# Performance work log

Measured on AMD Instinct MI355X. Metric: run time of the kernel, lower is better.

## Reference

```python
import jax, jax.numpy as jnp
import numpy as np

H = 768        # spanbert_out
WF = 20        # width_encoding_feature_size
MSW = 10       # max_span_width
TOP_RATIO = 0.4
MAX_ANTE = 50
DEPTH = 2      # coref_depth
D = 3 * H + WF # span_rep_size = 2324
NEG = -1e30


def setup_inputs() -> dict:
    key = jax.random.key(0)
    ks = jax.random.split(key, 12)
    W, G = 2048, 100
    seq = jax.random.normal(ks[0], (W, H), jnp.float32)
    sentence_map = jnp.sort(jax.random.randint(ks[1], (W,), 0, 64))
    gold_starts = jax.random.randint(ks[2], (G,), 0, W)
    gold_ends = jnp.clip(gold_starts + jax.random.randint(ks[3], (G,), 0, MSW), 0, W - 1)
    cluster_ids = jax.random.randint(ks[4], (G,), 0, 20)
    s = 0.02
    return {
        "sequence_output": seq,
        "W_alpha": jax.random.normal(ks[5], (H, 1), jnp.float32) * s,
        "b_alpha": jnp.zeros((1,), jnp.float32),
        "W_m": jax.random.normal(ks[6], (D, 1), jnp.float32) * s,
        "b_m": jnp.zeros((1,), jnp.float32),
        "W_c": jax.random.normal(ks[7], (D, D), jnp.float32) * s,
        "W_a": jax.random.normal(ks[8], (3 * D, 1), jnp.float32) * s,
        "b_a": jnp.zeros((1,), jnp.float32),
        "W_f": jax.random.normal(ks[9], (2 * D, D), jnp.float32) * s,
        "b_f": jnp.zeros((D,), jnp.float32),
        "width_feats": jax.random.normal(ks[10], (MSW, WF), jnp.float32) * s,
        "sentence_map": sentence_map,
        "gold_starts": gold_starts,
        "gold_ends": gold_ends,
        "cluster_ids": cluster_ids,
    }


def _forward(seq, W_alpha, b_alpha, W_m, b_m, W_c, W_a, b_a, W_f, b_f, width_feats,
             sentence_map, gold_starts, gold_ends, cluster_ids):
    W = seq.shape[0]
    # candidate spans: [W, MSW] -> flat [N], N = W*MSW
    cs = jnp.broadcast_to(jnp.arange(W)[:, None], (W, MSW)).reshape(-1)
    ce = (jnp.arange(W)[:, None] + jnp.arange(MSW)[None, :]).reshape(-1)
    ce_c = jnp.minimum(ce, W - 1)
    valid = (ce < W) & (sentence_map[cs] == sentence_map[ce_c])  # [N]

    # candidate cluster labels (get_candidate_labels): sum cluster ids of exact gold matches
    same_span = (cs[:, None] == gold_starts[None, :]) & (ce_c[:, None] == gold_ends[None, :])
    cand_cluster = jnp.sum(jnp.where(same_span, cluster_ids[None, :], 0), axis=1)  # [N]

    # span representations
    start_emb = seq[cs]                               # [N,H]
    end_emb = seq[ce_c]                               # [N,H]
    alphas = (seq @ W_alpha + b_alpha)[:, 0]          # [W]
    doc_range = jnp.arange(W)[None, :]
    mmask = (doc_range >= cs[:, None]) & (doc_range <= ce_c[:, None])  # [N,W]
    attn = jax.nn.softmax(jnp.where(mmask, alphas[None, :], NEG), axis=1)
    span_emb = attn @ seq                             # [N,H]
    widths = jnp.clip(ce_c - cs, 0, MSW - 1)          # width - 1
    rep = jnp.concatenate([start_emb, end_emb, span_emb, width_feats[widths]], axis=1)  # [N,D]

    # mention scoring + top-m pruning (masked_select replaced by -inf masking)
    mention_scores = (rep @ W_m + b_m)[:, 0]          # [N]
    masked_scores = jnp.where(valid, mention_scores, NEG)
    m = int(TOP_RATIO * W)
    _, top_idx = jax.lax.top_k(masked_scores, m)
    top_idx = jnp.sort(top_idx)
    top_rep = rep[top_idx]                            # [m,D]
    ts, te = cs[top_idx], ce_c[top_idx]
    tscore = mention_scores[top_idx]
    tcluster = cand_cluster[top_idx]

    # prune antecedents
    k = min(m, MAX_ANTE)
    offsets = jnp.arange(m)[:, None] - jnp.arange(m)[None, :]
    amask = offsets >= 1
    fast = tscore[:, None] + tscore[None, :] + jnp.where(amask, 0.0, NEG)
    fast = fast + (top_rep @ W_c) @ top_rep.T         # [m,m]
    _, top_ante = jax.lax.top_k(fast, k)              # [m,k]
    ta_mask = jnp.take_along_axis(amask, top_ante, axis=1)
    ta_fast = jnp.take_along_axis(fast, top_ante, axis=1)

    # iterative attention-weighted antecedent aggregation with gated update
    dummy = jnp.zeros((m, 1), seq.dtype)
    reps = top_rep
    scores_a = ta_fast
    for _ in range(DEPTH):
        ante_emb = reps[top_ante]                     # [m,k,D]
        tgt = reps[:, None, :]
        pair = jnp.concatenate(
            [jnp.broadcast_to(tgt, (m, k, D)), ante_emb, ante_emb * tgt], axis=2)  # [m,k,3D]
        slow = (pair @ W_a)[:, :, 0] + b_a[0]         # [m,k]
        scores_a = ta_fast + slow
        wts = jax.nn.softmax(jnp.concatenate([dummy, scores_a], axis=1), axis=1)  # [m,k+1]
        full = jnp.concatenate([reps[:, None, :], ante_emb], axis=1)              # [m,k+1,D]
        attended = jnp.sum(wts[:, :, None] * full, axis=1)                        # [m,D]
        f = jax.nn.sigmoid(jnp.concatenate([reps, attended], axis=1) @ W_f + b_f)
        reps = f * attended + (1.0 - f) * reps

    final_scores = jnp.concatenate([dummy, scores_a], axis=1)  # [m,k+1]

    # antecedent labels and marginal log-likelihood loss
    ante_cluster = jnp.where(ta_mask, tcluster[top_ante], -1)
    pairwise = (ante_cluster == tcluster[:, None]) & (tcluster > 0)[:, None]
    dummy_lab = ~jnp.any(pairwise, axis=1, keepdims=True)
    lab = jnp.concatenate([dummy_lab, pairwise], axis=1)
    gold_scores = jnp.where(lab, final_scores, NEG)
    loss = jnp.sum(jax.nn.logsumexp(final_scores, axis=1) - jax.nn.logsumexp(gold_scores, axis=1))
    return ts, te, top_ante, final_scores, loss


def reference(sequence_output, W_alpha, b_alpha, W_m, b_m, W_c, W_a, b_a, W_f, b_f,
              width_feats, sentence_map, gold_starts, gold_ends, cluster_ids):
    return _forward(sequence_output, W_alpha, b_alpha, W_m, b_m, W_c, W_a, b_a,
                    W_f, b_f, width_feats, sentence_map, gold_starts, gold_ends, cluster_ids)
```

## Files before the change

kernel.cpp:

```cpp
#include <hip/hip_runtime.h>
#include <cfloat>
#include <climits>
#include <math.h>

#define HD   768
#define MSW  10
#define WFK  20
#define DD   2324
#define K2   50
#define NEGF (-1e30f)

#define KPAD 2432
#define KAW  4864
#define MPAD 896
#define NPAD 2432

typedef __attribute__((ext_vector_type(8))) short    s8b;
typedef __attribute__((ext_vector_type(8))) unsigned short u16x8;
typedef __attribute__((ext_vector_type(4))) float    f32x4;

__device__ inline unsigned short f2bf(float f){
  unsigned u = __float_as_uint(f);
  unsigned r = (u + 0x7FFFu + ((u >> 16) & 1u)) >> 16;
  return (unsigned short)r;
}
__device__ inline float bf2f(unsigned short h){
  return __uint_as_float(((unsigned)h) << 16);
}

__device__ __forceinline__ void gload16(const unsigned short* g, void* l){
  __builtin_amdgcn_global_load_lds(
      (const __attribute__((address_space(1))) void*)g,
      (__attribute__((address_space(3))) void*)l, 16, 0, 0);
}

__device__ __forceinline__ int swz_col(int row, int col){
  return col ^ ((row & 7) << 3);
}

__device__ __forceinline__ void xcd_remap(int &bx, int &by, int &bz){
  int nwg  = (int)(gridDim.x*gridDim.y*gridDim.z);
  int orig = (int)(blockIdx.x + gridDim.x*(blockIdx.y + gridDim.y*blockIdx.z));
  int q = nwg >> 3, r = nwg & 7;
  int x8 = orig & 7, o8 = orig >> 3;
  int wg = (x8 < r ? x8*(q+1) : r*(q+1) + (x8-r)*q) + o8;
  bx = wg % (int)gridDim.x;
  int tmp = wg / (int)gridDim.x;
  by = tmp % (int)gridDim.y;
  bz = tmp / (int)gridDim.y;
}

__global__ void row_proj(const float* __restrict__ seq, const float* __restrict__ Wa,
                         const float* __restrict__ ba, const float* __restrict__ Wm,
                         float* alphas, float* p1, float* p2, float* p3, int W){
  int w = blockIdx.x; int tid = threadIdx.x;
  const float* row = seq + (size_t)w * HD;
  float s0=0.f, s1=0.f, s2=0.f, s3=0.f;
  for(int h=tid; h<HD; h+=256){
    float x = row[h];
    s0 += x * Wa[h];
    s1 += x * Wm[h];
    s2 += x * Wm[HD + h];
    s3 += x * Wm[2*HD + h];
  }
  __shared__ float r0[256], r1[256], r2[256], r3[256];
  r0[tid]=s0; r1[tid]=s1; r2[tid]=s2; r3[tid]=s3;
  __syncthreads();
  for(int st=128; st>0; st>>=1){
    if(tid<st){ r0[tid]+=r0[tid+st]; r1[tid]+=r1[tid+st]; r2[tid]+=r2[tid+st]; r3[tid]+=r3[tid+st]; }
    __syncthreads();
  }
  if(tid==0){ alphas[w]=r0[0]+ba[0]; p1[w]=r1[0]; p2[w]=r2[0]; p3[w]=r3[0]; }
}

__global__ void mention_kernel(const float* __restrict__ alphas, const float* __restrict__ p1,
                               const float* __restrict__ p2, const float* __restrict__ p3,
                               const float* __restrict__ wfeat, const float* __restrict__ Wm,
                               const float* __restrict__ bm,
                               const int* __restrict__ smap, const int* __restrict__ gs,
                               const int* __restrict__ ge, const int* __restrict__ cid, int G,
                               float* mscore, float* mmask, int* ccl, int W){
  int c = blockIdx.x*blockDim.x + threadIdx.x;
  int C = W * MSW;
  if(c >= C) return;
  int s = c / MSW, r = c - s*MSW;
  int e = s + r; int ec = min(e, W-1);
  int L = ec - s;
  bool valid = (e < W) && (smap[s] == smap[ec]);
  float maxa = -FLT_MAX;
  for(int j=0;j<=L;j++) maxa = fmaxf(maxa, alphas[s+j]);
  float sum=0.f, sdot=0.f;
  for(int j=0;j<=L;j++){ float ee = expf(alphas[s+j]-maxa); sum += ee; sdot += ee*p3[s+j]; }
  sdot /= sum;
  float wp=0.f;
  for(int f=0; f<WFK; f++) wp += wfeat[L*WFK+f] * Wm[3*HD+f];
  float ms = p1[s] + p2[ec] + sdot + wp + bm[0];
  mscore[c] = ms;
  mmask[c]  = valid ? ms : NEGF;
  int cc = 0;
  for(int g=0; g<G; g++) if(s==gs[g] && ec==ge[g]) cc += cid[g];
  ccl[c] = cc;
}

__device__ inline unsigned fkey(float f){
  unsigned b = __float_as_uint(f);
  return (b & 0x80000000u) ? ~b : (b | 0x80000000u);
}

__global__ __launch_bounds__(1024)
void select_kernel(const float* __restrict__ mmask, const float* __restrict__ mscore,
                   const int* __restrict__ ccl, int m, int C, int W,
                   int* top_idx, float* tscore, int* tclust,
                   float* out_ts, float* out_te){
  const int T = 1024;
  int tid = threadIdx.x;
  int chunk = (C + T - 1)/T;
  int lo = tid*chunk, hi = min(lo+chunk, C);
  int n = hi - lo; if(n < 0) n = 0;
  unsigned kb[32];
  for(int t=0;t<n;t++) kb[t] = fkey(mmask[lo+t]);

  __shared__ unsigned s_hist[256];
  __shared__ unsigned s_scan[1024];
  __shared__ unsigned s_pref;
  __shared__ int s_rem;
  if(tid==0){ s_pref=0u; s_rem=m; }
  __syncthreads();

  for(int b=3;b>=0;b--){
    if(tid<256) s_hist[tid]=0u;
    __syncthreads();
    unsigned pref = s_pref;
    unsigned msk = (b==3)?0u:(0xFFFFFFFFu << ((b+1)*8));
    for(int t=0;t<n;t++){
      unsigned u = kb[t];
      if((u & msk)==pref) atomicAdd(&s_hist[(u>>(b*8))&0xFFu], 1u);
    }
    __syncthreads();
    if(tid==0){
      int rem = s_rem; unsigned acc=0u; int bin;
      for(bin=255;bin>=1;bin--){
        unsigned h = s_hist[bin];
        if(acc + h >= (unsigned)rem) break;
        acc += h;
      }
      if(bin < 0) bin = 0;
      s_pref = pref | ((unsigned)bin << (b*8));
      s_rem = rem - (int)acc;
    }
    __syncthreads();
  }
  unsigned Tk = s_pref;
  int need = s_rem;

  unsigned nG=0, nE=0;
  for(int t=0;t<n;t++){ unsigned u=kb[t]; nG += (u>Tk)?1u:0u; nE += (u==Tk)?1u:0u; }

  s_scan[tid]=nE; __syncthreads();
  for(int off=1; off<T; off<<=1){
    unsigned x = (tid>=off)? s_scan[tid-off]:0u; __syncthreads();
    s_scan[tid]+=x; __syncthreads();
  }
  unsigned eqBase = s_scan[tid]-nE;
  __syncthreads();

  int takeLeft = need - (int)eqBase;
  int take = takeLeft<0?0:(takeLeft>(int)nE?(int)nE:takeLeft);
  unsigned selCnt = nG + (unsigned)take;

  s_scan[tid]=selCnt; __syncthreads();
  for(int off=1; off<T; off<<=1){
    unsigned x = (tid>=off)? s_scan[tid-off]:0u; __syncthreads();
    s_scan[tid]+=x; __syncthreads();
  }
  unsigned posBase = s_scan[tid]-selCnt;

  int pos = (int)posBase; int eq = (int)eqBase;
  for(int t=0;t<n;t++){
    unsigned u = kb[t];
    bool sel = false;
    if(u>Tk) sel=true;
    else if(u==Tk){ if(eq<need) sel=true; eq++; }
    if(sel){
      int c = lo+t;
      top_idx[pos] = c;
      int s = c/MSW, r = c - s*MSW; int e = min(s + r, W-1);
      tscore[pos] = mscore[c];
      tclust[pos] = ccl[c];
      out_ts[pos] = (float)s;
      out_te[pos] = (float)e;
      pos++;
    }
  }
}

__global__ void build_rep(const float* __restrict__ seq, const float* __restrict__ alphas,
                          const float* __restrict__ wfeat, const int* __restrict__ top_idx,
                          float* rep, int W){
  int i = blockIdx.x; int tid = threadIdx.x;
  int c = top_idx[i];
  int s = c/MSW, r = c - s*MSW; int ec = min(s + r, W-1); int L = ec - s;
  float wv[MSW];
  float maxa = -FLT_MAX;
  for(int j=0;j<=L;j++) maxa = fmaxf(maxa, alphas[s+j]);
  float sum = 0.f;
  for(int j=0;j<=L;j++){ wv[j] = expf(alphas[s+j]-maxa); sum += wv[j]; }
  float inv = 1.f/sum;
  float* o = rep + (size_t)i*DD;
  for(int d=tid; d<HD; d+=256){
    o[d]      = seq[(size_t)s*HD + d];
    o[HD+d]   = seq[(size_t)ec*HD + d];
    float sp = 0.f;
    for(int j=0;j<=L;j++) sp += wv[j]*seq[(size_t)(s+j)*HD + d];
    o[2*HD+d] = sp*inv;
  }
  for(int f=tid; f<WFK; f+=256) o[3*HD+f] = wfeat[L*WFK+f];
}

__global__ void conv_split(const float* __restrict__ src, int rows, int cols,
                           unsigned short* __restrict__ hi, unsigned short* __restrict__ lo,
                           float* __restrict__ ztgt, int zn){
  int idx = blockIdx.x*256 + threadIdx.x;
  if(idx >= MPAD*KPAD) return;
  if(idx < zn) ztgt[idx] = 0.f;
  int row = idx / KPAD, col = idx - row*KPAD;
  float v = (row < rows && col < cols) ? src[(size_t)row*cols + col] : 0.f;
  unsigned short h = f2bf(v);
  int w = row*KPAD + swz_col(row, col);
  hi[w] = h;
  lo[w] = f2bf(v - bf2f(h));
}

__global__ void conv_split_wcT(const float* __restrict__ Wc,
                               unsigned short* __restrict__ WtH, unsigned short* __restrict__ WtL){
  int n  = blockIdx.y*64 + threadIdx.x;
  int k8 = blockIdx.x*8;
  u16x8 vh, vl;
  #pragma unroll
  for(int j=0;j<8;j++){
    int k = k8 + j;
    float f = (n < DD && k < DD) ? Wc[(size_t)k*DD + n] : 0.f;
    unsigned short h = f2bf(f);
    vh[j] = h;
    vl[j] = f2bf(f - bf2f(h));
  }
  int k8s = swz_col(n, k8);
  *(u16x8*)(WtH + (size_t)n*KPAD + k8s) = vh;
  *(u16x8*)(WtL + (size_t)n*KPAD + k8s) = vl;
}

__global__ __launch_bounds__(256,2)
void gemm_split3_sk(const unsigned short* __restrict__ Ah, const unsigned short* __restrict__ Al,
                    const unsigned short* __restrict__ Bth, const unsigned short* __restrict__ Btl,
                    float* __restrict__ C, int M, int N, int ldc){
  __shared__ __align__(16) unsigned short sAh[128*64];
  __shared__ __align__(16) unsigned short sAl[128*64];
  __shared__ __align__(16) unsigned short sBh[128*64];
  __shared__ __align__(16) unsigned short sBl[128*64];
  int bx, by, bz; xcd_remap(bx, by, bz);
  int t = threadIdx.x;
  int row0 = by*128, col0 = bx*128;
  const int tiles = KPAD/64;
  int per = (tiles + (int)gridDim.z - 1)/(int)gridDim.z;
  int tb = min(bz*per, tiles), te = min(tb + per, tiles);
  if(tb >= te) return;
  int lane = t&63, w = t>>6;
  int wr = (w>>1)*64, wc = (w&1)*64;
  int quad = lane>>4, l15 = lane&15;
  int seg = lane&7;
  size_t ro = (size_t)(w*8 + (lane>>3));
  const unsigned short* gAh = Ah  + ((size_t)row0 + ro)*KPAD + seg*8;
  const unsigned short* gAl = Al  + ((size_t)row0 + ro)*KPAD + seg*8;
  const unsigned short* gBh = Bth + ((size_t)col0 + ro)*KPAD + seg*8;
  const unsigned short* gBl = Btl + ((size_t)col0 + ro)*KPAD + seg*8;
  const int lds0 = (w*8)*64;
  const int c0 = ((quad ^ (l15 & 7)) << 3);

  f32x4 acc[4][4];
  #pragma unroll
  for(int mi=0;mi<4;mi++)
    #pragma unroll
    for(int ni=0;ni<4;ni++) acc[mi][ni] = (f32x4){0.f,0.f,0.f,0.f};

  for(int kt=tb; kt<te; ++kt){
    size_t k0 = (size_t)kt*64;
    #pragma unroll
    for(int r=0;r<4;r++){
      size_t go = (size_t)(r*32)*KPAD + k0;
      int lo = lds0 + r*32*64;
      gload16(gAh + go, sAh + lo);
      gload16(gAl + go, sAl + lo);
      gload16(gBh + go, sBh + lo);
      gload16(gBl + go, sBl + lo);
    }
    __syncthreads();
    #pragma unroll
    for(int ks=0;ks<2;ks++){
      const int co = c0 ^ (ks<<5);
      s8b fah[4], fal[4], fbh[4], fbl[4];
      #pragma unroll
      for(int mi=0;mi<4;mi++){
        int ra = (wr+mi*16+l15)*64 + co;
        fah[mi] = *(const s8b*)&sAh[ra];
        fal[mi] = *(const s8b*)&sAl[ra];
      }
      #pragma unroll
      for(int ni=0;ni<4;ni++){
        int rb = (wc+ni*16+l15)*64 + co;
        fbh[ni] = *(const s8b*)&sBh[rb];
        fbl[ni] = *(const s8b*)&sBl[rb];
      }
      #pragma unroll
      for(int mi=0;mi<4;mi++)
        #pragma unroll
        for(int ni=0;ni<4;ni++){
          acc[mi][ni] = __builtin_amdgcn_mfma_f32_16x16x32_bf16(fah[mi], fbh[ni], acc[mi][ni], 0,0,0);
          acc[mi][ni] = __builtin_amdgcn_mfma_f32_16x16x32_bf16(fah[mi], fbl[ni], acc[mi][ni], 0,0,0);
          acc[mi][ni] = __builtin_amdgcn_mfma_f32_16x16x32_bf16(fal[mi], fbh[ni], acc[mi][ni], 0,0,0);
        }
    }
    __syncthreads();
  }

  #pragma unroll
  for(int ni=0;ni<4;ni++){
    int gn = col0 + wc + ni*16 + l15;
    if(gn >= N) continue;
    #pragma unroll
    for(int mi=0;mi<4;mi++){
      #pragma unroll
      for(int rg=0;rg<4;rg++){
        int gr = row0 + wr + mi*16 + quad*4 + rg;
        if(gr >= M) continue;
        atomicAdd(&C[(size_t)gr*ldc + gn], acc[mi][ni][rg]);
      }
    }
  }
}

__global__ __launch_bounds__(256,2)
void gemm_bf16_m97(const unsigned short* __restrict__ A, const unsigned short* __restrict__ Bt,
                   float* __restrict__ C, int M, int N, int ldc, int ldk, int tiles){
  __shared__ __align__(16) unsigned short sA[2][128*64];
  __shared__ __align__(16) unsigned short sB[2][128*64];
  int bx, by, bz; xcd_remap(bx, by, bz);
  int t = threadIdx.x;
  int row0 = by*128, col0 = bx*128;
  int per = (tiles + (int)gridDim.z - 1)/(int)gridDim.z;
  int tb = min(bz*per, tiles), te = min(tb + per, tiles);
  if(tb >= te) return;
  int lane = t&63, w = t>>6;
  int wr = (w>>1)*64, wc = (w&1)*64;
  int quad = lane>>4, l15 = lane&15;
  int seg = lane&7;
  size_t ro = (size_t)(w*8 + (lane>>3));
  const unsigned short* gA = A  + ((size_t)row0 + ro)*ldk + seg*8;
  const unsigned short* gB = Bt + ((size_t)col0 + ro)*ldk + seg*8;
  const int lds0 = (w*8)*64;
  const int c0 = ((quad ^ (l15 & 7)) << 3);

  f32x4 acc[4][4];
  #pragma unroll
  for(int mi=0;mi<4;mi++)
    #pragma unroll
    for(int ni=0;ni<4;ni++) acc[mi][ni] = (f32x4){0.f,0.f,0.f,0.f};

  auto STAGE = [&](int b, int kt){
    size_t k0 = (size_t)kt*64;
    #pragma unroll
    for(int r=0;r<4;r++){
      size_t go = (size_t)(r*32)*ldk + k0;
      int lo = lds0 + r*32*64;
      gload16(gA + go, &sA[b][lo]);
      gload16(gB + go, &sB[b][lo]);
    }
  };

  STAGE(0, tb);
  __syncthreads();
  int buf = 0;
  for(int kt=tb; kt<te; ++kt){
    if(kt+1 < te) STAGE(buf^1, kt+1);
    #pragma unroll
    for(int ks=0;ks<2;ks++){
      const int co = c0 ^ (ks<<5);
      s8b fa[4], fb[4];
      #pragma unroll
      for(int mi=0;mi<4;mi++) fa[mi] = *(const s8b*)&sA[buf][(wr+mi*16+l15)*64 + co];
      #pragma unroll
      for(int ni=0;ni<4;ni++) fb[ni] = *(const s8b*)&sB[buf][(wc+ni*16+l15)*64 + co];
      #pragma unroll
      for(int mi=0;mi<4;mi++)
        #pragma unroll
        for(int ni=0;ni<4;ni++)
          acc[mi][ni] = __builtin_amdgcn_mfma_f32_16x16x32_bf16(fa[mi], fb[ni], acc[mi][ni], 0,0,0);
    }
    __syncthreads();
    buf ^= 1;
  }

  #pragma unroll
  for(int ni=0;ni<4;ni++){
    int gn = col0 + wc + ni*16 + l15;
    if(gn >= N) continue;
    #pragma unroll
    for(int mi=0;mi<4;mi++){
      #pragma unroll
      for(int rg=0;rg<4;rg++){
        int gr = row0 + wr + mi*16 + quad*4 + rg;
        if(gr >= M) continue;
        atomicAdd(&C[(size_t)gr*ldc + gn], acc[mi][ni][rg]);
      }
    }
  }
}

#define NT 13
__global__ void topante_kernel(const float* __restrict__ tscore, const float* __restrict__ bilin,
                               int m, int* ante, float* tafast, float* out_ante){
  int i = blockIdx.x; int lane = threadIdx.x;
  float tsi = tscore[i];
  float v[NT];
  #pragma unroll
  for(int t=0;t<NT;t++){
    int j = lane + t*64;
    float f = -FLT_MAX;
    if(j < m){
      f = tsi + tscore[j];
      f += (j < i) ? 0.f : NEGF;
      f += bilin[(size_t)i*m + j];
    }
    v[t] = f;
  }
  unsigned consumed = 0u;
  int r_ante = 0; float r_fast = 0.f;
  for(int it=0; it<K2; ++it){
    float lv = -FLT_MAX; int li = m;
    #pragma unroll
    for(int t=0;t<NT;t++){
      bool live = ((consumed >> t) & 1u) == 0u;
      if(live && v[t] > lv){ lv = v[t]; li = lane + t*64; }
    }
    float bv = lv; int bi = li;
    #pragma unroll
    for(int off=32; off>0; off>>=1){
      float ov = __shfl_xor(bv, off);
      int   oi = __shfl_xor(bi, off);
      if(ov > bv || (ov == bv && oi < bi)){ bv = ov; bi = oi; }
    }
    if(bi < m && (bi & 63) == lane) consumed |= (1u << (bi >> 6));
    if(lane == it){ r_ante = bi; r_fast = bv; }
  }
  if(lane < K2){
    ante[(size_t)i*K2 + lane]   = r_ante;
    tafast[(size_t)i*K2 + lane] = r_fast;
    out_ante[(size_t)i*K2+lane] = (float)r_ante;
  }
}

__global__ void uv_kernel(const float* __restrict__ reps, const float* __restrict__ Wa3,
                          float* u, float* v, int m){
  int i = blockIdx.x; int tid = threadIdx.x;
  const float* rp = reps + (size_t)i*DD;
  float s1=0.f, s2=0.f;
  for(int d=tid; d<DD; d+=256){ float x = rp[d]; s1 += x*Wa3[d]; s2 += x*Wa3[DD+d]; }
  __shared__ float r1[256], r2[256];
  r1[tid]=s1; r2[tid]=s2; __syncthreads();
  for(int st=128; st>0; st>>=1){
    if(tid<st){ r1[tid]+=r1[tid+st]; r2[tid]+=r2[tid+st]; }
    __syncthreads();
  }
  if(tid==0){ u[i]=r1[0]; v[i]=r2[0]; }
}

__global__ __launch_bounds__(256)
void slow_dots(const float* __restrict__ cur, const float* __restrict__ Wa3,
               const float* __restrict__ u, const float* __restrict__ v,
               const int* __restrict__ ante, const float* __restrict__ tafast,
               const float* __restrict__ ba, float* __restrict__ sc, int m){
  int i  = blockIdx.y;
  int tq = blockIdx.x;
  int tid = threadIdx.x;
  int lane = tid & 63, w = tid >> 6;
  __shared__ __align__(16) float xi[DD];
  const float* ri = cur + (size_t)i*DD;
  for(int k=tid; k<DD; k+=256) xi[k] = ri[k]*Wa3[2*DD + k];
  __syncthreads();
  const float ui = u[i], b0 = ba[0];
  const int D4 = DD/4;
  const f32x4* xi4 = (const f32x4*)xi;
  int t0 = tq*10;
  for(int t=t0+w; t<t0+10; t+=4){
    int j = ante[(size_t)i*K2 + t];
    const f32x4* rj4 = (const f32x4*)(cur + (size_t)j*DD);
    float s = 0.f;
    for(int k=lane; k<D4; k+=64){
      f32x4 a = xi4[k], b = rj4[k];
      s += a[0]*b[0] + a[1]*b[1] + a[2]*b[2] + a[3]*b[3];
    }
    #pragma unroll
    for(int off=32; off>0; off>>=1) s += __shfl_xor(s, off);
    if(lane==0)
      sc[(size_t)i*K2 + t] = tafast[(size_t)i*K2 + t] + ui + v[j] + s + b0;
  }
}

__global__ __launch_bounds__(256)
void attend_d(const float* __restrict__ cur, const float* __restrict__ sc,
              const int* __restrict__ ante, float* __restrict__ att, int m){
  int i  = blockIdx.y;
  int ch = blockIdx.x;
  int tid = threadIdx.x;
  __shared__ float wts[K2+1];
  __shared__ float scs[K2];
  __shared__ int   js[K2];
  if(tid < K2){ scs[tid] = sc[(size_t)i*K2 + tid]; js[tid] = ante[(size_t)i*K2 + tid]; }
  __syncthreads();
  if(tid==0){
    float mx = 0.f;
    for(int t=0;t<K2;t++) mx = fmaxf(mx, scs[t]);
    float sum = expf(0.f - mx); wts[0] = sum;
    for(int t=0;t<K2;t++){ float e = expf(scs[t]-mx); wts[t+1]=e; sum += e; }
    float inv = 1.f/sum;
    for(int t=0;t<=K2;t++) wts[t] *= inv;
  }
  __syncthreads();
  const int D4 = DD/4;
  const int C4 = 146;
  int d4 = ch*C4 + tid;
  if(tid < C4 && d4 < D4){
    const f32x4* ri4 = (const f32x4*)(cur + (size_t)i*DD);
    f32x4 a = ri4[d4];
    float w0 = wts[0];
    a[0]*=w0; a[1]*=w0; a[2]*=w0; a[3]*=w0;
    for(int t=0;t<K2;t++){
      const f32x4* rj4 = (const f32x4*)(cur + (size_t)js[t]*DD);
      f32x4 b = rj4[d4];
      float wt = wts[t+1];
      a[0]+=wt*b[0]; a[1]+=wt*b[1]; a[2]+=wt*b[2]; a[3]+=wt*b[3];
    }
    ((f32x4*)(att + (size_t)i*DD))[d4] = a;
  }
}

__global__ void conv_acat(const float* __restrict__ cur, const float* __restrict__ att,
                          unsigned short* __restrict__ A,
                          float* __restrict__ nxt, int total, int m){
  int idx = blockIdx.x*256 + threadIdx.x;
  if(idx >= MPAD*KAW) return;
  if(idx < total) nxt[idx] = 0.f;
  int row = idx / KAW, col = idx - row*KAW;
  float v = 0.f;
  if(row < m){
    if(col < DD) v = cur[(size_t)row*DD + col];
    else if(col >= KPAD && col < KPAD + DD) v = att[(size_t)row*DD + (col - KPAD)];
  }
  A[row*KAW + swz_col(row, col)] = f2bf(v);
}

__global__ void conv_wf(const float* __restrict__ Wf, unsigned short* __restrict__ Bt){
  int n  = blockIdx.y*64 + threadIdx.x;
  int k8 = blockIdx.x*8;
  int s  = (k8 >= KPAD) ? 1 : 0;
  int kk = k8 - s*KPAD;
  u16x8 v;
  #pragma unroll
  for(int j=0;j<8;j++){
    int k = kk + j;
    float f = (n < DD && k < DD) ? Wf[(size_t)(s*DD + k)*DD + n] : 0.f;
    v[j] = f2bf(f);
  }
  int k8s = swz_col(n, k8);
  *(u16x8*)(Bt + (size_t)n*KAW + k8s) = v;
}

__global__ void gate_update(const float* __restrict__ bfv, const float* __restrict__ att,
                            const float* __restrict__ cur, float* __restrict__ nxt, int total){
  int idx = blockIdx.x*256 + threadIdx.x;
  if(idx >= total) return;
  int col = idx % DD;
  float pre = nxt[idx] + bfv[col];
  float g = 1.f/(1.f + expf(-pre));
  nxt[idx] = g*att[idx] + (1.f - g)*cur[idx];
}

__global__ void final_loss(const float* __restrict__ sc, const int* __restrict__ ante,
                           const int* __restrict__ tclust, float* out_fs, float* row_loss, int m){
  int i = blockIdx.x*blockDim.x + threadIdx.x;
  if(i >= m) return;
  int tci = tclust[i];
  unsigned long long labm = 0ull;
  bool anyp = false;
  float mx = 0.f;
  float mg = -FLT_MAX;
  for(int t=0;t<K2;t++){
    float v = sc[(size_t)i*K2 + t];
    mx = fmaxf(mx, v);
    int j = ante[(size_t)i*K2 + t];
    bool mk = (j < i);
    int ac = mk ? tclust[j] : -1;
    bool p = (ac == tci) && (tci > 0);
    if(p){ labm |= (1ull << (t+1)); anyp = true; mg = fmaxf(mg, v); }
  }
  if(!anyp){ labm |= 1ull; mg = 0.f; }
  float s1 = expf(0.f - mx);
  float s2 = (labm & 1ull) ? expf(0.f - mg) : 0.f;
  float* o = out_fs + (size_t)i*(K2+1);
  o[0] = 0.f;
  for(int t=0;t<K2;t++){
    float v = sc[(size_t)i*K2 + t];
    o[t+1] = v;
    s1 += expf(v - mx);
    if(labm & (1ull << (t+1))) s2 += expf(v - mg);
  }
  row_loss[i] = (mx + logf(s1)) - (mg + logf(s2));
}

__global__ void loss_sum(const float* __restrict__ row_loss, float* out, int m){
  int tid = threadIdx.x;
  float s = 0.f;
  for(int i=tid; i<m; i+=256) s += row_loss[i];
  __shared__ float red[256];
  red[tid]=s; __syncthreads();
  for(int st=128; st>0; st>>=1){ if(tid<st) red[tid]+=red[tid+st]; __syncthreads(); }
  if(tid==0) out[0] = red[0];
}

extern "C" void kernel_launch(void* const* d_in, const int* in_sizes, int n_in,
                              void* d_out, int out_size, void* d_ws, size_t ws_size,
                              hipStream_t stream){
  const int W = in_sizes[11];
  const int G = in_sizes[12];
  const int C = W * MSW;
  const int m = (int)(0.4 * (double)W);

  const float* seq   = (const float*)d_in[0];
  const float* Wal   = (const float*)d_in[1];
  const float* bal   = (const float*)d_in[2];
  const float* Wm    = (const float*)d_in[3];
  const float* bm    = (const float*)d_in[4];
  const float* Wc    = (const float*)d_in[5];
  const float* WaA   = (const float*)d_in[6];
  const float* baA   = (const float*)d_in[7];
  const float* Wf    = (const float*)d_in[8];
  const float* bf    = (const float*)d_in[9];
  const float* wfeat = (const float*)d_in[10];
  const int*   smap  = (const int*)d_in[11];
  const int*   gs    = (const int*)d_in[12];
  const int*   ge    = (const int*)d_in[13];
  const int*   cid   = (const int*)d_in[14];
  float* out = (float*)d_out;

  char* ws = (char*)d_ws;
  size_t off = 0;
  auto alloc = [&](size_t bytes)->char*{
    char* p = ws + off;
    off += (bytes + 255) & ~(size_t)255;
    return p;
  };
  const size_t PLANE  = (size_t)MPAD*KPAD*2;
  const size_t WPLANE = (size_t)NPAD*KPAD*2;

  float* alphas  = (float*)alloc((size_t)W*4);
  float* p1      = (float*)alloc((size_t)W*4);
  float* p2      = (float*)alloc((size_t)W*4);
  float* p3      = (float*)alloc((size_t)W*4);
  float* mscore  = (float*)alloc((size_t)C*4);
  float* mmask   = (float*)alloc((size_t)C*4);
  int*   ccl     = (int*)  alloc((size_t)C*4);
  int*   top_idx = (int*)  alloc((size_t)m*4);
  float* tscore  = (float*)alloc((size_t)m*4);
  int*   tclust  = (int*)  alloc((size_t)m*4);
  float* B1      = (float*)alloc((size_t)m*DD*4);
  float* B2      = (float*)alloc((size_t)m*DD*4);
  float* B3      = (float*)alloc((size_t)m*DD*4);
  float* bilin   = (float*)alloc((size_t)m*m*4);
  int*   ante    = (int*)  alloc((size_t)m*K2*4);
  float* tafast  = (float*)alloc((size_t)m*K2*4);
  float* uB      = (float*)alloc((size_t)m*4);
  float* vB      = (float*)alloc((size_t)m*4);
  float* scB     = (float*)alloc((size_t)m*K2*4);
  float* rloss   = (float*)alloc((size_t)m*4);
  char* regionA = alloc(2*PLANE);
  unsigned short* RepH  = (unsigned short*)regionA;
  unsigned short* RepL  = (unsigned short*)(regionA + PLANE);
  unsigned short* Acat  = (unsigned short*)regionA;
  char* regionB = alloc(2*WPLANE);
  unsigned short* WtH  = (unsigned short*)regionB;
  unsigned short* WtL  = (unsigned short*)(regionB + WPLANE);
  unsigned short* A2H  = (unsigned short*)regionB;
  unsigned short* A2L  = (unsigned short*)(regionB + PLANE);
  unsigned short* BtWf = (unsigned short*)regionB;

  float* out_ts   = out;
  float* out_te   = out + m;
  float* out_ante = out + 2*m;
  float* out_fs   = out + 2*m + (size_t)m*K2;
  float* out_loss = out + 2*m + (size_t)m*K2 + (size_t)m*(K2+1);

  row_proj<<<W, 256, 0, stream>>>(seq, Wal, bal, Wm, alphas, p1, p2, p3, W);
  mention_kernel<<<(C+255)/256, 256, 0, stream>>>(alphas, p1, p2, p3, wfeat, Wm, bm,
                                                  smap, gs, ge, cid, G,
                                                  mscore, mmask, ccl, W);
  select_kernel<<<1, 1024, 0, stream>>>(mmask, mscore, ccl, m, C, W,
                                        top_idx, tscore, tclust, out_ts, out_te);
  build_rep<<<m, 256, 0, stream>>>(seq, alphas, wfeat, top_idx, B1, W);
  {
    const int NEL = MPAD*KPAD;
    conv_split<<<(NEL+255)/256, 256, 0, stream>>>(B1, m, DD, RepH, RepL, B2, m*DD);
    dim3 gw(KPAD/8, NPAD/64);
    conv_split_wcT<<<gw, 64, 0, stream>>>(Wc, WtH, WtL);
    dim3 g1(NPAD/128, MPAD/128, 3);
    gemm_split3_sk<<<g1, 256, 0, stream>>>(RepH, RepL, WtH, WtL, B2, m, DD, DD);
    conv_split<<<(NEL+255)/256, 256, 0, stream>>>(B2, m, DD, A2H, A2L, bilin, m*m);
    dim3 g2(MPAD/128, MPAD/128, 10);
    gemm_split3_sk<<<g2, 256, 0, stream>>>(A2H, A2L, RepH, RepL, bilin, m, m, m);
  }
  topante_kernel<<<m, 64, 0, stream>>>(tscore, bilin, m, ante, tafast, out_ante);
  {
    dim3 g(KAW/8, NPAD/64);
    conv_wf<<<g, 64, 0, stream>>>(Wf, BtWf);
  }

  float* cur = B1; float* nxt = B2;
  const int total = m * DD;
  for(int depth=0; depth<2; depth++){
    uv_kernel<<<m, 256, 0, stream>>>(cur, WaA, uB, vB, m);
    slow_dots<<<dim3(5, m), 256, 0, stream>>>(cur, WaA, uB, vB, ante, tafast, baA, scB, m);
    attend_d<<<dim3(4, m), 256, 0, stream>>>(cur, scB, ante, B3, m);
    conv_acat<<<(MPAD*KAW+255)/256, 256, 0, stream>>>(cur, B3, Acat, nxt, total, m);
    dim3 gg(NPAD/128, MPAD/128, 3);
    gemm_bf16_m97<<<gg, 256, 0, stream>>>(Acat, BtWf, nxt, m, DD, DD, KAW, KAW/64);
    gate_update<<<(total+255)/256, 256, 0, stream>>>(bf, B3, cur, nxt, total);
    float* t = cur; cur = nxt; nxt = t;
  }

  final_loss<<<(m+255)/256, 256, 0, stream>>>(scB, ante, tclust, out_fs, rloss, m);
  loss_sum<<<1, 256, 0, stream>>>(rloss, out_loss, m);
}
```

Measured before the change: 718.2 us.

## Use wave-shuffle scans in top-k select and fuse gate with uv dots and loss reduction

```diff
diff --git a/kernel.cpp b/kernel.cpp
--- a/kernel.cpp
+++ b/kernel.cpp
@@ -114,6 +114,7 @@
                    float* out_ts, float* out_te){
   const int T = 1024;
   int tid = threadIdx.x;
+  int lane = tid & 63, wid = tid >> 6;
   int chunk = (C + T - 1)/T;
   int lo = tid*chunk, hi = min(lo+chunk, C);
   int n = hi - lo; if(n < 0) n = 0;
@@ -121,7 +122,8 @@
   for(int t=0;t<n;t++) kb[t] = fkey(mmask[lo+t]);
 
   __shared__ unsigned s_hist[256];
-  __shared__ unsigned s_scan[1024];
+  __shared__ unsigned s_w4[4];
+  __shared__ unsigned s_w16[16];
   __shared__ unsigned s_pref;
   __shared__ int s_rem;
   if(tid==0){ s_pref=0u; s_rem=m; }
@@ -137,16 +139,30 @@
       if((u & msk)==pref) atomicAdd(&s_hist[(u>>(b*8))&0xFFu], 1u);
     }
     __syncthreads();
-    if(tid==0){
-      int rem = s_rem; unsigned acc=0u; int bin;
-      for(bin=255;bin>=1;bin--){
-        unsigned h = s_hist[bin];
-        if(acc + h >= (unsigned)rem) break;
-        acc += h;
+    unsigned x = 0, hb = 0;
+    if(tid < 256){
+      hb = s_hist[255 - tid];
+      x = hb;
+      #pragma unroll
+      for(int off=1; off<64; off<<=1){
+        unsigned y = __shfl_up(x, off);
+        if(lane >= off) x += y;
       }
-      if(bin < 0) bin = 0;
-      s_pref = pref | ((unsigned)bin << (b*8));
-      s_rem = rem - (int)acc;
+      if(lane==63) s_w4[wid] = x;
+    }
+    __syncthreads();
+    if(tid < 256){
+      unsigned add = 0;
+      for(int q=0; q<wid; q++) add += s_w4[q];
+      unsigned P = x + add;
+      int bbin = 255 - tid;
+      unsigned rem = (unsigned)s_rem;
+      unsigned SSb1 = P - hb;
+      bool win = (bbin == 0) ? (SSb1 < rem) : (P >= rem && SSb1 < rem);
+      if(win){
+        s_pref = pref | ((unsigned)bbin << (b*8));
+        s_rem  = (int)(rem - SSb1);
+      }
     }
     __syncthreads();
   }
@@ -156,24 +172,52 @@
   unsigned nG=0, nE=0;
   for(int t=0;t<n;t++){ unsigned u=kb[t]; nG += (u>Tk)?1u:0u; nE += (u==Tk)?1u:0u; }
 
-  s_scan[tid]=nE; __syncthreads();
-  for(int off=1; off<T; off<<=1){
-    unsigned x = (tid>=off)? s_scan[tid-off]:0u; __syncthreads();
-    s_scan[tid]+=x; __syncthreads();
-  }
-  unsigned eqBase = s_scan[tid]-nE;
-  __syncthreads();
+  unsigned x1 = nE;
+  #pragma unroll
+  for(int off=1; off<64; off<<=1){
+    unsigned y = __shfl_up(x1, off);
+    if(lane >= off) x1 += y;
+  }
+  if(lane==63) s_w16[wid] = x1;
+  __syncthreads();
+  if(wid==0){
+    unsigned wv = (lane<16) ? s_w16[lane] : 0u;
+    #pragma unroll
+    for(int off=1; off<16; off<<=1){
+      unsigned y = __shfl_up(wv, off);
+      if(lane >= off) wv += y;
+    }
+    if(lane<16) s_w16[lane] = wv;
+  }
+  __syncthreads();
+  unsigned incl1 = x1 + (wid>0 ? s_w16[wid-1] : 0u);
+  unsigned eqBase = incl1 - nE;
 
   int takeLeft = need - (int)eqBase;
   int take = takeLeft<0?0:(takeLeft>(int)nE?(int)nE:takeLeft);
   unsigned selCnt = nG + (unsigned)take;
 
-  s_scan[tid]=selCnt; __syncthreads();
-  for(int off=1; off<T; off<<=1){
-    unsigned x = (tid>=off)? s_scan[tid-off]:0u; __syncthreads();
-    s_scan[tid]+=x; __syncthreads();
-  }
-  unsigned posBase = s_scan[tid]-selCnt;
+  __syncthreads();
+  unsigned x2 = selCnt;
+  #pragma unroll
+  for(int off=1; off<64; off<<=1){
+    unsigned y = __shfl_up(x2, off);
+    if(lane >= off) x2 += y;
+  }
+  if(lane==63) s_w16[wid] = x2;
+  __syncthreads();
+  if(wid==0){
+    unsigned wv = (lane<16) ? s_w16[lane] : 0u;
+    #pragma unroll
+    for(int off=1; off<16; off<<=1){
+      unsigned y = __shfl_up(wv, off);
+      if(lane >= off) wv += y;
+    }
+    if(lane<16) s_w16[lane] = wv;
+  }
+  __syncthreads();
+  unsigned incl2 = x2 + (wid>0 ? s_w16[wid-1] : 0u);
+  unsigned posBase = incl2 - selCnt;
 
   int pos = (int)posBase; int eq = (int)eqBase;
   for(int t=0;t<n;t++){
@@ -574,56 +618,70 @@
   *(u16x8*)(Bt + (size_t)n*KAW + k8s) = v;
 }
 
-__global__ void gate_update(const float* __restrict__ bfv, const float* __restrict__ att,
-                            const float* __restrict__ cur, float* __restrict__ nxt, int total){
-  int idx = blockIdx.x*256 + threadIdx.x;
-  if(idx >= total) return;
-  int col = idx % DD;
-  float pre = nxt[idx] + bfv[col];
-  float g = 1.f/(1.f + expf(-pre));
-  nxt[idx] = g*att[idx] + (1.f - g)*cur[idx];
+__global__ void gate_uv(const float* __restrict__ bfv, const float* __restrict__ att,
+                        const float* __restrict__ cur, float* __restrict__ nxt,
+                        const float* __restrict__ Wa3, float* u, float* v,
+                        float* __restrict__ out_loss, int m){
+  int i = blockIdx.x; int tid = threadIdx.x;
+  if(i==0 && tid==0) out_loss[0] = 0.f;
+  const size_t base = (size_t)i*DD;
+  float s1=0.f, s2=0.f;
+  for(int d=tid; d<DD; d+=256){
+    float pre = nxt[base+d] + bfv[d];
+    float g = 1.f/(1.f + expf(-pre));
+    float val = g*att[base+d] + (1.f - g)*cur[base+d];
+    nxt[base+d] = val;
+    s1 += val*Wa3[d]; s2 += val*Wa3[DD+d];
+  }
+  __shared__ float r1[256], r2[256];
+  r1[tid]=s1; r2[tid]=s2; __syncthreads();
+  for(int st=128; st>0; st>>=1){
+    if(tid<st){ r1[tid]+=r1[tid+st]; r2[tid]+=r2[tid+st]; }
+    __syncthreads();
+  }
+  if(tid==0){ u[i]=r1[0]; v[i]=r2[0]; }
 }
 
 __global__ void final_loss(const float* __restrict__ sc, const int* __restrict__ ante,
-                           const int* __restrict__ tclust, float* out_fs, float* row_loss, int m){
+                           const int* __restrict__ tclust, float* out_fs,
+                           float* __restrict__ out_loss, int m){
   int i = blockIdx.x*blockDim.x + threadIdx.x;
-  if(i >= m) return;
-  int tci = tclust[i];
-  unsigned long long labm = 0ull;
-  bool anyp = false;
-  float mx = 0.f;
-  float mg = -FLT_MAX;
-  for(int t=0;t<K2;t++){
-    float v = sc[(size_t)i*K2 + t];
-    mx = fmaxf(mx, v);
-    int j = ante[(size_t)i*K2 + t];
-    bool mk = (j < i);
-    int ac = mk ? tclust[j] : -1;
-    bool p = (ac == tci) && (tci > 0);
-    if(p){ labm |= (1ull << (t+1)); anyp = true; mg = fmaxf(mg, v); }
-  }
-  if(!anyp){ labm |= 1ull; mg = 0.f; }
-  float s1 = expf(0.f - mx);
-  float s2 = (labm & 1ull) ? expf(0.f - mg) : 0.f;
-  float* o = out_fs + (size_t)i*(K2+1);
-  o[0] = 0.f;
-  for(int t=0;t<K2;t++){
-    float v = sc[(size_t)i*K2 + t];
-    o[t+1] = v;
-    s1 += expf(v - mx);
-    if(labm & (1ull << (t+1))) s2 += expf(v - mg);
-  }
-  row_loss[i] = (mx + logf(s1)) - (mg + logf(s2));
-}
-
-__global__ void loss_sum(const float* __restrict__ row_loss, float* out, int m){
-  int tid = threadIdx.x;
-  float s = 0.f;
-  for(int i=tid; i<m; i+=256) s += row_loss[i];
+  float L = 0.f;
+  if(i < m){
+    int tci = tclust[i];
+    unsigned long long labm = 0ull;
+    bool anyp = false;
+    float mx = 0.f;
+    float mg = -FLT_MAX;
+    for(int t=0;t<K2;t++){
+      float v = sc[(size_t)i*K2 + t];
+      mx = fmaxf(mx, v);
+      int j = ante[(size_t)i*K2 + t];
+      bool mk = (j < i);
+      int ac = mk ? tclust[j] : -1;
+      bool p = (ac == tci) && (tci > 0);
+      if(p){ labm |= (1ull << (t+1)); anyp = true; mg = fmaxf(mg, v); }
+    }
+    if(!anyp){ labm |= 1ull; mg = 0.f; }
+    float s1 = expf(0.f - mx);
+    float s2 = (labm & 1ull) ? expf(0.f - mg) : 0.f;
+    float* o = out_fs + (size_t)i*(K2+1);
+    o[0] = 0.f;
+    for(int t=0;t<K2;t++){
+      float v = sc[(size_t)i*K2 + t];
+      o[t+1] = v;
+      s1 += expf(v - mx);
+      if(labm & (1ull << (t+1))) s2 += expf(v - mg);
+    }
+    L = (mx + logf(s1)) - (mg + logf(s2));
+  }
   __shared__ float red[256];
-  red[tid]=s; __syncthreads();
-  for(int st=128; st>0; st>>=1){ if(tid<st) red[tid]+=red[tid+st]; __syncthreads(); }
-  if(tid==0) out[0] = red[0];
+  red[threadIdx.x] = L; __syncthreads();
+  for(int st=128; st>0; st>>=1){
+    if(threadIdx.x < st) red[threadIdx.x] += red[threadIdx.x+st];
+    __syncthreads();
+  }
+  if(threadIdx.x==0) atomicAdd(out_loss, red[0]);
 }
 
 extern "C" void kernel_launch(void* const* d_in, const int* in_sizes, int n_in,
@@ -691,6 +749,7 @@
   unsigned short* A2H  = (unsigned short*)regionB;
   unsigned short* A2L  = (unsigned short*)(regionB + PLANE);
   unsigned short* BtWf = (unsigned short*)regionB;
+  (void)rloss;
 
   float* out_ts   = out;
   float* out_te   = out + m;
@@ -724,17 +783,16 @@
 
   float* cur = B1; float* nxt = B2;
   const int total = m * DD;
+  uv_kernel<<<m, 256, 0, stream>>>(cur, WaA, uB, vB, m);
   for(int depth=0; depth<2; depth++){
-    uv_kernel<<<m, 256, 0, stream>>>(cur, WaA, uB, vB, m);
     slow_dots<<<dim3(5, m), 256, 0, stream>>>(cur, WaA, uB, vB, ante, tafast, baA, scB, m);
     attend_d<<<dim3(4, m), 256, 0, stream>>>(cur, scB, ante, B3, m);
     conv_acat<<<(MPAD*KAW+255)/256, 256, 0, stream>>>(cur, B3, Acat, nxt, total, m);
     dim3 gg(NPAD/128, MPAD/128, 3);
     gemm_bf16_m97<<<gg, 256, 0, stream>>>(Acat, BtWf, nxt, m, DD, DD, KAW, KAW/64);
-    gate_update<<<(total+255)/256, 256, 0, stream>>>(bf, B3, cur, nxt, total);
+    gate_uv<<<m, 256, 0, stream>>>(bf, B3, cur, nxt, WaA, uB, vB, out_loss, m);
     float* t = cur; cur = nxt; nxt = t;
   }
 
-  final_loss<<<(m+255)/256, 256, 0, stream>>>(scB, ante, tclust, out_fs, rloss, m);
-  loss_sum<<<1, 256, 0, stream>>>(rloss, out_loss, m);
-}
+  final_loss<<<(m+255)/256, 256, 0, stream>>>(scB, ante, tclust, out_fs, out_loss, m);
+}
```

Result: no change. 710.3 us (-1.1%).
